# Kernel optimization log

Measured on AMD Instinct MI355X. Metric: run time of the kernel, lower is better.

Reference implementation:

```python
import jax, jax.numpy as jnp
import numpy as np

NUM_EXPERT = 64
TOP_K = 2
N_TOKENS = 16384
H_DIM = 4096


def setup_inputs() -> dict:
    key = jax.random.key(0)
    k1, k2, k3 = jax.random.split(key, 3)
    x = jax.random.normal(k1, (N_TOKENS, H_DIM), dtype=jnp.float32)
    # nn.Linear(h_dim, num_expert): weight [E, H], bias [E]
    W = jax.random.normal(k2, (NUM_EXPERT, H_DIM), dtype=jnp.float32) * (1.0 / np.sqrt(H_DIM))
    b = jax.random.normal(k3, (NUM_EXPERT,), dtype=jnp.float32) * 0.01
    return {"x": x, "W": W, "b": b}


def reference(x, W, b):
    # gating linear: [N, H] @ [H, E] + [E] -> [N, E]
    router_logits = x @ W.T + b
    # softmax over experts in float32 (matches dtype=torch.float)
    router_probs = jax.nn.softmax(router_logits.astype(jnp.float32), axis=1)
    # top-k over experts (values sorted descending, like torch.topk)
    router_weights, selected_experts_idx = jax.lax.top_k(router_probs, TOP_K)
    # renormalize via second softmax over the top_k dim (dim=1 of [N, K])
    router_weights = jax.nn.softmax(router_weights, axis=1).astype(x.dtype)
    # one-hot expert mask [N, K, E] -> permute(2,1,0) -> [E, K, N]
    expert_mask = jax.nn.one_hot(selected_experts_idx, NUM_EXPERT, dtype=jnp.int32)
    expert_mask = jnp.transpose(expert_mask, (2, 1, 0))
    return router_logits, router_weights, selected_experts_idx, expert_mask
```

## Files before the change

kernel.cpp:

```cpp
#include <hip/hip_runtime.h>
#include <hip/hip_bf16.h>
#include <math.h>

#define H_DIM 4096
#define N_EXP 64
#define N_TOK 16384
#define BM    32
#define KB    64
#define NCHUNK (H_DIM / KB)
#define MARGIN 1e-3f
#define SLOT_BYTES 24576

typedef __attribute__((ext_vector_type(8))) short short8v;
typedef __attribute__((ext_vector_type(4))) float float4v;

__device__ __forceinline__ unsigned short bf16_rn(float f) {
    unsigned u = __builtin_bit_cast(unsigned, f);
    u += 0x7FFFu + ((u >> 16) & 1u);
    return (unsigned short)(u >> 16);
}
__device__ __forceinline__ float bf16_hi_f32(unsigned u) {
    return __builtin_bit_cast(float, u & 0xFFFF0000u);
}
__device__ __forceinline__ void gload_lds16(const void* g, void* l) {
    __builtin_amdgcn_global_load_lds(
        (const __attribute__((address_space(1))) unsigned int*)g,
        (__attribute__((address_space(3))) unsigned int*)l, 16, 0, 0);
}

__global__ __launch_bounds__(256)
void wconvert_kernel(const float* __restrict__ W,
                     unsigned short* __restrict__ wh,
                     unsigned short* __restrict__ wm,
                     int* __restrict__ counter) {
    int i = blockIdx.x * 256 + threadIdx.x;
    if (i == 0) *counter = 0;
    float w = W[i];
    unsigned u = __builtin_bit_cast(unsigned, w);
    wh[i] = (unsigned short)(u >> 16);
    wm[i] = bf16_rn(w - bf16_hi_f32(u));
}

__global__ __launch_bounds__(256, 2)
void router_mfma_kernel(const float* __restrict__ x,
                        const unsigned short* __restrict__ wh,
                        const unsigned short* __restrict__ wm,
                        const float* __restrict__ bias,
                        float* __restrict__ logits,
                        float* __restrict__ wout,
                        float* __restrict__ iout,
                        int* __restrict__ counter,
                        int* __restrict__ list) {
    __shared__ char smem[3 * SLOT_BYTES];
    float* olds = (float*)smem;

    const int tid  = threadIdx.x;
    const int lane = tid & 63;
    const int wid  = __builtin_amdgcn_readfirstlane(tid >> 6);
    const int tok0 = blockIdx.x * BM;

    const int q    = lane >> 4;
    const int e15  = lane & 15;
    const int mt   = wid & 1;
    const int eg   = wid >> 1;
    const int arow = mt * 16 + e15;
    const int er0  = eg * 32 + e15;
    const int er1  = eg * 32 + 16 + e15;

    float4v acc0 = {0.f, 0.f, 0.f, 0.f};
    float4v acc1 = {0.f, 0.f, 0.f, 0.f};

    auto stage = [&](int slot, int c) {
        const int kc = c * KB;
        char* base = smem + slot * SLOT_BYTES;
#pragma unroll
        for (int i = 0; i < 2; ++i) {
            int idx = i * 256 + tid;
            int row = idx >> 4, u = idx & 15;
            int us  = u ^ (row & 15);
            const float* src = x + (size_t)(tok0 + row) * H_DIM + kc + us * 4;
            void* dst = base + (size_t)(i * 256 + wid * 64) * 16;
            gload_lds16(src, dst);
        }
#pragma unroll
        for (int j = 0; j < 4; ++j) {
            int idx = j * 256 + tid;
            int s = idx >> 9, e = (idx >> 3) & 63, u = idx & 7;
            int us = u ^ (e & 7);
            const unsigned short* wsrc = s ? wm : wh;
            const unsigned short* src  = wsrc + (size_t)e * H_DIM + kc + us * 8;
            void* dst = base + 8192 + (size_t)(j * 256 + wid * 64) * 16;
            gload_lds16(src, dst);
        }
    };

    auto compute = [&](int slot) {
        const char* xc = smem + slot * SLOT_BYTES;
        const char* wc = xc + 8192;
#pragma unroll
        for (int t = 0; t < 2; ++t) {
            float f[8];
#pragma unroll
            for (int h = 0; h < 2; ++h) {
                int u = (t * 8 + q * 2 + h) ^ e15;
                float4 a = *(const float4*)(xc + (size_t)(arow * 16 + u) * 16);
                f[h * 4 + 0] = a.x; f[h * 4 + 1] = a.y;
                f[h * 4 + 2] = a.z; f[h * 4 + 3] = a.w;
            }
            short8v ah, am;
#pragma unroll
            for (int j = 0; j < 8; ++j) {
                unsigned u = __builtin_bit_cast(unsigned, f[j]);
                ah[j] = (short)(u >> 16);
                am[j] = (short)bf16_rn(f[j] - bf16_hi_f32(u));
            }
            int up = (t * 4 + q) ^ (e15 & 7);
            short8v bh0 = *(const short8v*)(wc + (size_t)(0   + er0 * 8 + up) * 16);
            short8v bh1 = *(const short8v*)(wc + (size_t)(0   + er1 * 8 + up) * 16);
            short8v bm0 = *(const short8v*)(wc + (size_t)(512 + er0 * 8 + up) * 16);
            short8v bm1 = *(const short8v*)(wc + (size_t)(512 + er1 * 8 + up) * 16);

            acc0 = __builtin_amdgcn_mfma_f32_16x16x32_bf16(ah, bh0, acc0, 0, 0, 0);
            acc1 = __builtin_amdgcn_mfma_f32_16x16x32_bf16(ah, bh1, acc1, 0, 0, 0);
            acc0 = __builtin_amdgcn_mfma_f32_16x16x32_bf16(am, bh0, acc0, 0, 0, 0);
            acc1 = __builtin_amdgcn_mfma_f32_16x16x32_bf16(am, bh1, acc1, 0, 0, 0);
            acc0 = __builtin_amdgcn_mfma_f32_16x16x32_bf16(ah, bm0, acc0, 0, 0, 0);
            acc1 = __builtin_amdgcn_mfma_f32_16x16x32_bf16(ah, bm1, acc1, 0, 0, 0);
            acc0 = __builtin_amdgcn_mfma_f32_16x16x32_bf16(am, bm0, acc0, 0, 0, 0);
            acc1 = __builtin_amdgcn_mfma_f32_16x16x32_bf16(am, bm1, acc1, 0, 0, 0);
        }
    };

    stage(0, 0);
    stage(1, 1);
    for (int c = 0; c < NCHUNK; ++c) {
        __builtin_amdgcn_s_barrier();
        if (c + 2 < NCHUNK) {
            stage((c + 2) % 3, c + 2);
            asm volatile("s_waitcnt vmcnt(12)" ::: "memory");
        } else if (c + 1 < NCHUNK) {
            asm volatile("s_waitcnt vmcnt(6)" ::: "memory");
        } else {
            asm volatile("s_waitcnt vmcnt(0)" ::: "memory");
        }
        __builtin_amdgcn_s_barrier();
        compute(c % 3);
    }
    __syncthreads();

    float bv0 = bias[er0], bv1 = bias[er1];
#pragma unroll
    for (int r = 0; r < 4; ++r) {
        int trow = mt * 16 + q * 4 + r;
        float v0 = acc0[r] + bv0;
        float v1 = acc1[r] + bv1;
        logits[(size_t)(tok0 + trow) * N_EXP + er0] = v0;
        logits[(size_t)(tok0 + trow) * N_EXP + er1] = v1;
        olds[trow * 66 + er0] = v0;
        olds[trow * 66 + er1] = v1;
    }
    __syncthreads();

#pragma unroll
    for (int it = 0; it < 8; ++it) {
        const int nl = wid * 8 + it;
        const int n  = tok0 + nl;
        float l = olds[nl * 66 + lane];

        float v1 = l; int i1 = lane;
#pragma unroll
        for (int off = 32; off >= 1; off >>= 1) {
            float ov = __shfl_xor(v1, off);
            int   oi = __shfl_xor(i1, off);
            if (ov > v1 || (ov == v1 && oi < i1)) { v1 = ov; i1 = oi; }
        }
        float l2 = (lane == i1) ? -INFINITY : l;
        float v2 = l2; int i2 = lane;
#pragma unroll
        for (int off = 32; off >= 1; off >>= 1) {
            float ov = __shfl_xor(v2, off);
            int   oi = __shfl_xor(i2, off);
            if (ov > v2 || (ov == v2 && oi < i2)) { v2 = ov; i2 = oi; }
        }
        float l3 = (lane == i1 || lane == i2) ? -INFINITY : l;
        float v3 = l3;
#pragma unroll
        for (int off = 32; off >= 1; off >>= 1)
            v3 = fmaxf(v3, __shfl_xor(v3, off));

        float Z = expf(l - v1);
#pragma unroll
        for (int off = 32; off >= 1; off >>= 1) Z += __shfl_xor(Z, off);

        if (lane == 0) {
            float p1 = 1.0f / Z;
            float p2 = expf(v2 - v1) / Z;
            float t  = expf(p2 - p1);
            wout[2 * n + 0] = 1.0f / (1.0f + t);
            wout[2 * n + 1] = t / (1.0f + t);
            iout[2 * n + 0] = (float)i1;
            iout[2 * n + 1] = (float)i2;
            if ((v1 - v2 < MARGIN) || (v2 - v3 < MARGIN)) {
                int sidx = atomicAdd(counter, 1);
                list[sidx] = n;
            }
        }
    }
}

__global__ __launch_bounds__(256)
void router_logits_f32(const float* __restrict__ x,
                       const float* __restrict__ W,
                       const float* __restrict__ bias,
                       float* __restrict__ logits) {
    __shared__ float4 wlds[32 * 64];
    __shared__ float4 xlds[32][32];
    const int tid = threadIdx.x;
    const int lane = tid & 63;
    const int wid = __builtin_amdgcn_readfirstlane(tid >> 6);
    const int tok0b = blockIdx.x * 32;
    const int trow0 = wid * 8;
    float acc[8];
#pragma unroll
    for (int t = 0; t < 8; ++t) acc[t] = 0.0f;
    for (int kc = 0; kc < H_DIM; kc += 128) {
        __syncthreads();
#pragma unroll
        for (int i = 0; i < 8; ++i) {
            int idx = tid + i * 256;
            int se = idx >> 5, sj = idx & 31;
            float4 v = *(const float4*)(W + (size_t)se * H_DIM + kc + sj * 4);
            wlds[sj * 64 + (se ^ (sj & 7))] = v;
        }
#pragma unroll
        for (int i = 0; i < 4; ++i) {
            int idx = tid + i * 256;
            int row = idx >> 5, col = idx & 31;
            xlds[row][col] = *(const float4*)(x + (size_t)(tok0b + row) * H_DIM + kc + col * 4);
        }
        __syncthreads();
#pragma unroll 4
        for (int jg = 0; jg < 32; ++jg) {
            float4 w = wlds[jg * 64 + (lane ^ (jg & 7))];
#pragma unroll
            for (int t = 0; t < 8; ++t) {
                float4 xv = xlds[trow0 + t][jg];
                acc[t] = fmaf(w.x, xv.x, acc[t]);
                acc[t] = fmaf(w.y, xv.y, acc[t]);
                acc[t] = fmaf(w.z, xv.z, acc[t]);
                acc[t] = fmaf(w.w, xv.w, acc[t]);
            }
        }
    }
    float bv = bias[lane];
#pragma unroll
    for (int t = 0; t < 8; ++t)
        logits[(size_t)(tok0b + trow0 + t) * N_EXP + lane] = acc[t] + bv;
}

__global__ __launch_bounds__(256)
void topk_kernel(const float* __restrict__ logits,
                 float* __restrict__ wout,
                 float* __restrict__ iout) {
    const int lane = threadIdx.x & 63;
    const int wid  = threadIdx.x >> 6;
    const int wg   = blockIdx.x * 4 + wid;
#pragma unroll
    for (int it = 0; it < 4; ++it) {
        const int n = wg * 4 + it;
        float l = logits[(size_t)n * N_EXP + lane];
        float v1 = l; int i1 = lane;
#pragma unroll
        for (int off = 32; off >= 1; off >>= 1) {
            float ov = __shfl_xor(v1, off);
            int   oi = __shfl_xor(i1, off);
            if (ov > v1 || (ov == v1 && oi < i1)) { v1 = ov; i1 = oi; }
        }
        float l2 = (lane == i1) ? -INFINITY : l;
        float v2 = l2; int i2 = lane;
#pragma unroll
        for (int off = 32; off >= 1; off >>= 1) {
            float ov = __shfl_xor(v2, off);
            int   oi = __shfl_xor(i2, off);
            if (ov > v2 || (ov == v2 && oi < i2)) { v2 = ov; i2 = oi; }
        }
        float Z = expf(l - v1);
#pragma unroll
        for (int off = 32; off >= 1; off >>= 1) Z += __shfl_xor(Z, off);
        if (lane == 0) {
            float p1 = 1.0f / Z;
            float p2 = expf(v2 - v1) / Z;
            float t  = expf(p2 - p1);
            wout[2 * n + 0] = 1.0f / (1.0f + t);
            wout[2 * n + 1] = t / (1.0f + t);
            iout[2 * n + 0] = (float)i1;
            iout[2 * n + 1] = (float)i2;
        }
    }
}

__global__ __launch_bounds__(256)
void fixup_kernel(const float* __restrict__ x,
                  const float* __restrict__ W,
                  const float* __restrict__ bias,
                  float* __restrict__ wout,
                  float* __restrict__ iout,
                  const int* __restrict__ counter,
                  const int* __restrict__ list) {
    __shared__ float plds[4][64];
    __shared__ float llds[64];
    int cnt = counter[0];
    if (cnt > N_TOK) cnt = N_TOK;
    const int e = threadIdx.x & 63;
    const int s = threadIdx.x >> 6;
    for (int it = blockIdx.x; it < cnt; it += 128) {
        int n = list[it];
        const float4* xr = (const float4*)(x + (size_t)n * H_DIM) + s * 256;
        const float4* wr = (const float4*)(W + (size_t)e * H_DIM) + s * 256;
        float p = 0.f;
#pragma unroll 8
        for (int j = 0; j < 256; ++j) {
            float4 a = xr[j], w = wr[j];
            p = fmaf(a.x, w.x, p); p = fmaf(a.y, w.y, p);
            p = fmaf(a.z, w.z, p); p = fmaf(a.w, w.w, p);
        }
        plds[s][e] = p;
        __syncthreads();
        if (threadIdx.x < 64)
            llds[e] = ((plds[0][e] + plds[1][e]) + (plds[2][e] + plds[3][e])) + bias[e];
        __syncthreads();
        if (threadIdx.x == 0) {
            float v1 = -INFINITY, v2 = -INFINITY;
            int i1 = 0, i2 = 0;
            for (int i = 0; i < 64; ++i) {
                float li = llds[i];
                if (li > v1)      { v2 = v1; i2 = i1; v1 = li; i1 = i; }
                else if (li > v2) { v2 = li; i2 = i; }
            }
            float Z = 0.0f;
            for (int i = 0; i < 64; ++i) Z += expf(llds[i] - v1);
            float p1 = 1.0f / Z;
            float p2 = expf(v2 - v1) / Z;
            float t  = expf(p2 - p1);
            wout[2 * n + 0] = 1.0f / (1.0f + t);
            wout[2 * n + 1] = t / (1.0f + t);
            iout[2 * n + 0] = (float)i1;
            iout[2 * n + 1] = (float)i2;
        }
        __syncthreads();
    }
}

__global__ __launch_bounds__(256)
void mask_kernel(const float* __restrict__ iout,
                 float* __restrict__ mask) {
    int gid = blockIdx.x * 256 + threadIdx.x;
    int n   = gid & (N_TOK - 1);
    int ek  = gid >> 14;
    float idxf = iout[(size_t)n * 2 + (ek & 1)];
    mask[gid] = (idxf == (float)(ek >> 1)) ? 1.0f : 0.0f;
}

extern "C" void kernel_launch(void* const* d_in, const int* in_sizes, int n_in,
                              void* d_out, int out_size, void* d_ws, size_t ws_size,
                              hipStream_t stream) {
    const float* x  = (const float*)d_in[0];
    const float* W  = (const float*)d_in[1];
    const float* b  = (const float*)d_in[2];

    float* out    = (float*)d_out;
    float* logits = out;
    float* wout   = logits + (size_t)N_TOK * 64;
    float* iout   = wout   + (size_t)N_TOK * 2;
    float* mask   = iout   + (size_t)N_TOK * 2;

    const size_t wsplit = (size_t)N_EXP * H_DIM;
    const size_t need   = 2 * wsplit * sizeof(unsigned short) + 4 + (size_t)N_TOK * 4;
    if (ws_size >= need) {
        unsigned short* wh = (unsigned short*)d_ws;
        unsigned short* wm = wh + wsplit;
        int* counter = (int*)((char*)d_ws + 2 * wsplit * sizeof(unsigned short));
        int* list    = counter + 1;
        wconvert_kernel<<<(int)(wsplit / 256), 256, 0, stream>>>(W, wh, wm, counter);
        router_mfma_kernel<<<N_TOK / BM, 256, 0, stream>>>(x, wh, wm, b, logits,
                                                           wout, iout, counter, list);
        fixup_kernel<<<128, 256, 0, stream>>>(x, W, b, wout, iout, counter, list);
    } else {
        router_logits_f32<<<N_TOK / 32, 256, 0, stream>>>(x, W, b, logits);
        topk_kernel<<<N_TOK / 16, 256, 0, stream>>>(logits, wout, iout);
    }
    mask_kernel<<<(N_EXP * 2 * N_TOK) / 256, 256, 0, stream>>>(iout, mask);
}
```

Before: 151.3 us.

## Split x to bf16 hi/lo once at staging via register prefetch

x is no longer copied into LDS as fp32 by direct global-to-LDS loads. Each thread now loads its x fragment into registers, splits it into bf16 high and low parts once, and writes both to LDS, so the compute loop reads ready MFMA operands. Previously every wave that read an x row redid the split, and this change removes that duplicated conversion and halves LDS traffic for x. In exchange it adds register pressure and extra waits, and the loop is hand-unrolled by two with manual vmcnt and lgkmcnt accounting that could be fragile.

New measurement: 152.6 us. No clear change (+0.8%).

```diff
diff --git a/kernel.cpp b/kernel.cpp
--- a/kernel.cpp
+++ b/kernel.cpp
@@ -67,21 +67,35 @@
     const int er0  = eg * 32 + e15;
     const int er1  = eg * 32 + 16 + e15;
 
+    const int srow = tid >> 3;
+    const int skg  = tid & 7;
+    const float* xsrc = x + (size_t)(tok0 + srow) * H_DIM + skg * 8;
+    const int xoff = (skg * 32 + srow) * 16;
+
     float4v acc0 = {0.f, 0.f, 0.f, 0.f};
     float4v acc1 = {0.f, 0.f, 0.f, 0.f};
 
-    auto stage = [&](int slot, int c) {
+    auto issue_x = [&](float4& g0, float4& g1, int c) {
+        const float* s = xsrc + c * KB;
+        g0 = *(const float4*)(s);
+        g1 = *(const float4*)(s + 4);
+    };
+    auto write_x = [&](float4 g0, float4 g1, int slot) {
+        float f[8] = {g0.x, g0.y, g0.z, g0.w, g1.x, g1.y, g1.z, g1.w};
+        short8v xh8, xm8;
+#pragma unroll
+        for (int j = 0; j < 8; ++j) {
+            unsigned u = __builtin_bit_cast(unsigned, f[j]);
+            xh8[j] = (short)(u >> 16);
+            xm8[j] = (short)bf16_rn(f[j] - bf16_hi_f32(u));
+        }
+        char* base = smem + slot * SLOT_BYTES;
+        *(short8v*)(base + xoff)        = xh8;
+        *(short8v*)(base + 4096 + xoff) = xm8;
+    };
+    auto issue_w = [&](int slot, int c) {
         const int kc = c * KB;
-        char* base = smem + slot * SLOT_BYTES;
-#pragma unroll
-        for (int i = 0; i < 2; ++i) {
-            int idx = i * 256 + tid;
-            int row = idx >> 4, u = idx & 15;
-            int us  = u ^ (row & 15);
-            const float* src = x + (size_t)(tok0 + row) * H_DIM + kc + us * 4;
-            void* dst = base + (size_t)(i * 256 + wid * 64) * 16;
-            gload_lds16(src, dst);
-        }
+        char* wdst = smem + slot * SLOT_BYTES + 8192;
 #pragma unroll
         for (int j = 0; j < 4; ++j) {
             int idx = j * 256 + tid;
@@ -89,36 +103,22 @@
             int us = u ^ (e & 7);
             const unsigned short* wsrc = s ? wm : wh;
             const unsigned short* src  = wsrc + (size_t)e * H_DIM + kc + us * 8;
-            void* dst = base + 8192 + (size_t)(j * 256 + wid * 64) * 16;
-            gload_lds16(src, dst);
+            gload_lds16(src, wdst + (size_t)(j * 256 + wid * 64) * 16);
         }
     };
-
     auto compute = [&](int slot) {
         const char* xc = smem + slot * SLOT_BYTES;
         const char* wc = xc + 8192;
 #pragma unroll
         for (int t = 0; t < 2; ++t) {
-            float f[8];
-#pragma unroll
-            for (int h = 0; h < 2; ++h) {
-                int u = (t * 8 + q * 2 + h) ^ e15;
-                float4 a = *(const float4*)(xc + (size_t)(arow * 16 + u) * 16);
-                f[h * 4 + 0] = a.x; f[h * 4 + 1] = a.y;
-                f[h * 4 + 2] = a.z; f[h * 4 + 3] = a.w;
-            }
-            short8v ah, am;
-#pragma unroll
-            for (int j = 0; j < 8; ++j) {
-                unsigned u = __builtin_bit_cast(unsigned, f[j]);
-                ah[j] = (short)(u >> 16);
-                am[j] = (short)bf16_rn(f[j] - bf16_hi_f32(u));
-            }
+            int au = ((t * 4 + q) * 32 + arow) * 16;
+            short8v ah = *(const short8v*)(xc + au);
+            short8v am = *(const short8v*)(xc + 4096 + au);
             int up = (t * 4 + q) ^ (e15 & 7);
-            short8v bh0 = *(const short8v*)(wc + (size_t)(0   + er0 * 8 + up) * 16);
-            short8v bh1 = *(const short8v*)(wc + (size_t)(0   + er1 * 8 + up) * 16);
-            short8v bm0 = *(const short8v*)(wc + (size_t)(512 + er0 * 8 + up) * 16);
-            short8v bm1 = *(const short8v*)(wc + (size_t)(512 + er1 * 8 + up) * 16);
+            short8v bh0 = *(const short8v*)(wc + (size_t)(er0 * 8 + up) * 16);
+            short8v bh1 = *(const short8v*)(wc + (size_t)(er1 * 8 + up) * 16);
+            short8v bm0 = *(const short8v*)(wc + 8192 + (size_t)(er0 * 8 + up) * 16);
+            short8v bm1 = *(const short8v*)(wc + 8192 + (size_t)(er1 * 8 + up) * 16);
 
             acc0 = __builtin_amdgcn_mfma_f32_16x16x32_bf16(ah, bh0, acc0, 0, 0, 0);
             acc1 = __builtin_amdgcn_mfma_f32_16x16x32_bf16(ah, bh1, acc1, 0, 0, 0);
@@ -131,21 +131,40 @@
         }
     };
 
-    stage(0, 0);
-    stage(1, 1);
-    for (int c = 0; c < NCHUNK; ++c) {
+    float4 xrA0, xrA1, xrB0, xrB1;
+
+    issue_x(xrA0, xrA1, 0);
+    issue_w(0, 0);
+    write_x(xrA0, xrA1, 0);
+    issue_x(xrB0, xrB1, 1);
+    issue_w(1, 1);
+    asm volatile("s_waitcnt vmcnt(6)" ::: "memory");
+
+    for (int c = 0; c < NCHUNK - 2; c += 2) {
+        asm volatile("s_waitcnt lgkmcnt(0)" ::: "memory");
         __builtin_amdgcn_s_barrier();
-        if (c + 2 < NCHUNK) {
-            stage((c + 2) % 3, c + 2);
-            asm volatile("s_waitcnt vmcnt(12)" ::: "memory");
-        } else if (c + 1 < NCHUNK) {
-            asm volatile("s_waitcnt vmcnt(6)" ::: "memory");
-        } else {
-            asm volatile("s_waitcnt vmcnt(0)" ::: "memory");
-        }
+        write_x(xrB0, xrB1, (c + 1) % 3);
+        issue_x(xrA0, xrA1, c + 2);
+        issue_w((c + 2) % 3, c + 2);
+        asm volatile("s_waitcnt vmcnt(6)" ::: "memory");
+        compute(c % 3);
+
+        asm volatile("s_waitcnt lgkmcnt(0)" ::: "memory");
         __builtin_amdgcn_s_barrier();
-        compute(c % 3);
-    }
+        write_x(xrA0, xrA1, (c + 2) % 3);
+        issue_x(xrB0, xrB1, c + 3);
+        issue_w((c + 3) % 3, c + 3);
+        asm volatile("s_waitcnt vmcnt(6)" ::: "memory");
+        compute((c + 1) % 3);
+    }
+    asm volatile("s_waitcnt lgkmcnt(0)" ::: "memory");
+    __builtin_amdgcn_s_barrier();
+    write_x(xrB0, xrB1, (NCHUNK - 1) % 3);
+    asm volatile("s_waitcnt vmcnt(0)" ::: "memory");
+    compute((NCHUNK - 2) % 3);
+    asm volatile("s_waitcnt lgkmcnt(0)" ::: "memory");
+    __builtin_amdgcn_s_barrier();
+    compute((NCHUNK - 1) % 3);
     __syncthreads();
 
     float bv0 = bias[er0], bv1 = bias[er1];
```

## Split router GEMM across 512 threads with one expert tile per wave, double-buffered

Applied to the files above, without the earlier changes.

The router kernel now launches 512 threads per block, so each of 8 waves computes a single 16x16 expert tile instead of two. The LDS pipeline drops from triple to double buffering, which shrinks shared memory and allows more resident blocks. The intent is more waves in flight to hide global-load latency. The cost is a shallower prefetch depth and more barrier participants per block.

Measured after the change: 148.5 us (median of 2 runs). No clear change (-1.9%).

```diff
diff --git a/kernel.cpp b/kernel.cpp
--- a/kernel.cpp
+++ b/kernel.cpp
@@ -41,7 +41,7 @@
     wm[i] = bf16_rn(w - bf16_hi_f32(u));
 }
 
-__global__ __launch_bounds__(256, 2)
+__global__ __launch_bounds__(512, 4)
 void router_mfma_kernel(const float* __restrict__ x,
                         const unsigned short* __restrict__ wh,
                         const unsigned short* __restrict__ wm,
@@ -51,7 +51,7 @@
                         float* __restrict__ iout,
                         int* __restrict__ counter,
                         int* __restrict__ list) {
-    __shared__ char smem[3 * SLOT_BYTES];
+    __shared__ char smem[2 * SLOT_BYTES];
     float* olds = (float*)smem;
 
     const int tid  = threadIdx.x;
@@ -64,33 +64,26 @@
     const int mt   = wid & 1;
     const int eg   = wid >> 1;
     const int arow = mt * 16 + e15;
-    const int er0  = eg * 32 + e15;
-    const int er1  = eg * 32 + 16 + e15;
-
-    float4v acc0 = {0.f, 0.f, 0.f, 0.f};
-    float4v acc1 = {0.f, 0.f, 0.f, 0.f};
-
-    auto stage = [&](int slot, int c) {
-        const int kc = c * KB;
+    const int er   = eg * 16 + e15;
+
+    float4v acc = {0.f, 0.f, 0.f, 0.f};
+
+    auto stage = [&](int slot, int kc) {
         char* base = smem + slot * SLOT_BYTES;
-#pragma unroll
-        for (int i = 0; i < 2; ++i) {
-            int idx = i * 256 + tid;
-            int row = idx >> 4, u = idx & 15;
+        {
+            int row = tid >> 4, u = tid & 15;
             int us  = u ^ (row & 15);
             const float* src = x + (size_t)(tok0 + row) * H_DIM + kc + us * 4;
-            void* dst = base + (size_t)(i * 256 + wid * 64) * 16;
-            gload_lds16(src, dst);
-        }
-#pragma unroll
-        for (int j = 0; j < 4; ++j) {
-            int idx = j * 256 + tid;
+            gload_lds16(src, base + (size_t)(wid * 64) * 16);
+        }
+#pragma unroll
+        for (int j = 0; j < 2; ++j) {
+            int idx = j * 512 + tid;
             int s = idx >> 9, e = (idx >> 3) & 63, u = idx & 7;
             int us = u ^ (e & 7);
             const unsigned short* wsrc = s ? wm : wh;
             const unsigned short* src  = wsrc + (size_t)e * H_DIM + kc + us * 8;
-            void* dst = base + 8192 + (size_t)(j * 256 + wid * 64) * 16;
-            gload_lds16(src, dst);
+            gload_lds16(src, base + 8192 + (size_t)(j * 512 + wid * 64) * 16);
         }
     };
 
@@ -102,7 +95,7 @@
             float f[8];
 #pragma unroll
             for (int h = 0; h < 2; ++h) {
-                int u = (t * 8 + q * 2 + h) ^ e15;
+                int u = (t * 8 + q * 2 + h) ^ (arow & 15);
                 float4 a = *(const float4*)(xc + (size_t)(arow * 16 + u) * 16);
                 f[h * 4 + 0] = a.x; f[h * 4 + 1] = a.y;
                 f[h * 4 + 2] = a.z; f[h * 4 + 3] = a.w;
@@ -115,55 +108,43 @@
                 am[j] = (short)bf16_rn(f[j] - bf16_hi_f32(u));
             }
             int up = (t * 4 + q) ^ (e15 & 7);
-            short8v bh0 = *(const short8v*)(wc + (size_t)(0   + er0 * 8 + up) * 16);
-            short8v bh1 = *(const short8v*)(wc + (size_t)(0   + er1 * 8 + up) * 16);
-            short8v bm0 = *(const short8v*)(wc + (size_t)(512 + er0 * 8 + up) * 16);
-            short8v bm1 = *(const short8v*)(wc + (size_t)(512 + er1 * 8 + up) * 16);
-
-            acc0 = __builtin_amdgcn_mfma_f32_16x16x32_bf16(ah, bh0, acc0, 0, 0, 0);
-            acc1 = __builtin_amdgcn_mfma_f32_16x16x32_bf16(ah, bh1, acc1, 0, 0, 0);
-            acc0 = __builtin_amdgcn_mfma_f32_16x16x32_bf16(am, bh0, acc0, 0, 0, 0);
-            acc1 = __builtin_amdgcn_mfma_f32_16x16x32_bf16(am, bh1, acc1, 0, 0, 0);
-            acc0 = __builtin_amdgcn_mfma_f32_16x16x32_bf16(ah, bm0, acc0, 0, 0, 0);
-            acc1 = __builtin_amdgcn_mfma_f32_16x16x32_bf16(ah, bm1, acc1, 0, 0, 0);
-            acc0 = __builtin_amdgcn_mfma_f32_16x16x32_bf16(am, bm0, acc0, 0, 0, 0);
-            acc1 = __builtin_amdgcn_mfma_f32_16x16x32_bf16(am, bm1, acc1, 0, 0, 0);
+            short8v bh = *(const short8v*)(wc + (size_t)(er * 8 + up) * 16);
+            short8v bm = *(const short8v*)(wc + 8192 + (size_t)(er * 8 + up) * 16);
+
+            acc = __builtin_amdgcn_mfma_f32_16x16x32_bf16(ah, bh, acc, 0, 0, 0);
+            acc = __builtin_amdgcn_mfma_f32_16x16x32_bf16(am, bh, acc, 0, 0, 0);
+            acc = __builtin_amdgcn_mfma_f32_16x16x32_bf16(ah, bm, acc, 0, 0, 0);
+            acc = __builtin_amdgcn_mfma_f32_16x16x32_bf16(am, bm, acc, 0, 0, 0);
         }
     };
 
     stage(0, 0);
-    stage(1, 1);
     for (int c = 0; c < NCHUNK; ++c) {
         __builtin_amdgcn_s_barrier();
-        if (c + 2 < NCHUNK) {
-            stage((c + 2) % 3, c + 2);
-            asm volatile("s_waitcnt vmcnt(12)" ::: "memory");
-        } else if (c + 1 < NCHUNK) {
-            asm volatile("s_waitcnt vmcnt(6)" ::: "memory");
+        if (c + 1 < NCHUNK) {
+            stage((c + 1) & 1, (c + 1) * KB);
+            asm volatile("s_waitcnt vmcnt(3)" ::: "memory");
         } else {
             asm volatile("s_waitcnt vmcnt(0)" ::: "memory");
         }
         __builtin_amdgcn_s_barrier();
-        compute(c % 3);
+        compute(c & 1);
     }
     __syncthreads();
 
-    float bv0 = bias[er0], bv1 = bias[er1];
+    float bv = bias[er];
 #pragma unroll
     for (int r = 0; r < 4; ++r) {
         int trow = mt * 16 + q * 4 + r;
-        float v0 = acc0[r] + bv0;
-        float v1 = acc1[r] + bv1;
-        logits[(size_t)(tok0 + trow) * N_EXP + er0] = v0;
-        logits[(size_t)(tok0 + trow) * N_EXP + er1] = v1;
-        olds[trow * 66 + er0] = v0;
-        olds[trow * 66 + er1] = v1;
+        float v = acc[r] + bv;
+        logits[(size_t)(tok0 + trow) * N_EXP + er] = v;
+        olds[trow * 66 + er] = v;
     }
     __syncthreads();
 
 #pragma unroll
-    for (int it = 0; it < 8; ++it) {
-        const int nl = wid * 8 + it;
+    for (int it = 0; it < 4; ++it) {
+        const int nl = wid * 4 + it;
         const int n  = tok0 + nl;
         float l = olds[nl * 66 + lane];
 
@@ -382,7 +363,7 @@
         int* counter = (int*)((char*)d_ws + 2 * wsplit * sizeof(unsigned short));
         int* list    = counter + 1;
         wconvert_kernel<<<(int)(wsplit / 256), 256, 0, stream>>>(W, wh, wm, counter);
-        router_mfma_kernel<<<N_TOK / BM, 256, 0, stream>>>(x, wh, wm, b, logits,
+        router_mfma_kernel<<<N_TOK / BM, 512, 0, stream>>>(x, wh, wm, b, logits,
                                                            wout, iout, counter, list);
         fixup_kernel<<<128, 256, 0, stream>>>(x, W, b, wout, iout, counter, list);
     } else {
```
